# Optimization experiments

Measured on AMD Instinct MI355X. Metric: run time of the kernel, lower is better.

## Reference

```python
import jax, jax.numpy as jnp
import numpy as np
from jax import lax

N = 4096        # number of nodes (= number of hyperedges)
F_DIM = 256     # feature_dim
E_DIM = 128     # embed_dim
K = 9           # hardcoded k_neig in forward


def setup_inputs() -> dict:
    key = jax.random.key(0)
    ks = jax.random.split(key, 10)
    x = jax.random.normal(ks[0], (N, F_DIM), jnp.float32)
    # distance/similarity matrix; continuous values avoid argsort tie ambiguity
    XY_Adj = jax.random.uniform(ks[1], (N, N), jnp.float32)

    def unif(k, shape, fan_out):  # torch HGNN_conv init: U(-1/sqrt(out), 1/sqrt(out))
        s = 1.0 / np.sqrt(fan_out)
        return jax.random.uniform(k, shape, jnp.float32, -s, s)

    W10 = unif(ks[2], (F_DIM, E_DIM), E_DIM); b10 = unif(ks[3], (E_DIM,), E_DIM)
    W11 = unif(ks[4], (E_DIM, E_DIM), E_DIM); b11 = unif(ks[5], (E_DIM,), E_DIM)
    W20 = unif(ks[6], (E_DIM, E_DIM), E_DIM); b20 = unif(ks[7], (E_DIM,), E_DIM)
    W21 = unif(ks[8], (E_DIM, F_DIM), F_DIM); b21 = unif(ks[9], (F_DIM,), F_DIM)
    return {"x": x, "XY_Adj": XY_Adj,
            "W10": W10, "b10": b10, "W11": W11, "b11": b11,
            "W20": W20, "b20": b20, "W21": W21, "b21": b21}


def _build_G(dis, k):
    """Vectorized construct_H_with_KNN_from_distance + _generate_G_from_H.
    Picks the k LARGEST entries per row (original does reversed argsort),
    forces the center node into its own hyperedge, builds binary H [N,N]
    (rows=nodes, cols=hyperedges), then G = DV^-1/2 H DE^-1 H^T DV^-1/2 (W=I)."""
    n = dis.shape[0]
    centers = jnp.arange(n)
    dis = jnp.where(jnp.eye(n, dtype=bool), 0.0, dis)  # zero the diagonal
    _, idx = lax.top_k(dis, k)                         # [N, k] descending per row
    has_center = (idx == centers[:, None]).any(axis=1)
    idx = idx.at[:, k - 1].set(jnp.where(has_center, idx[:, k - 1], centers))
    H = jnp.zeros((n, n), dis.dtype).at[idx, centers[:, None]].set(1.0)
    DV = H.sum(axis=1)                                 # node degrees (>=1)
    DE = H.sum(axis=0)                                 # hyperedge degrees (=k)
    dv2 = DV ** -0.5
    left = dv2[:, None] * H * (1.0 / DE)[None, :]      # DV^-1/2 H DE^-1
    G = left @ (H.T * dv2[None, :])                    # ... H^T DV^-1/2
    return G


def _hgnn(x, G, W1, b1, W2, b2):
    # HGNN: relu(G(xW1+b1)) -> dropout (identity in eval) -> G(hW2+b2)
    h = jax.nn.relu(G @ (x @ W1 + b1))
    return G @ (h @ W2 + b2)


def reference(x, XY_Adj, W10, b10, W11, b11, W20, b20, W21, b21):
    G = _build_G(XY_Adj, K)
    x1 = jax.nn.relu(_hgnn(x, G, W10, b10, W11, b11))
    x2 = jax.nn.relu(_hgnn(x1, G, W20, b20, W21, b21))
    return (x, x1, x2)
```

## Files before the change

### kernel.cpp

```cpp
#include <hip/hip_runtime.h>

#define N_NODES 4096
#define KNN 9
#define CAPS 128
#define CAPE 32
#define THRESH 0.99f
#define GEMMB 1024

__device__ __forceinline__ bool vi_greater(float av, int aj, float bv, int bj) {
  return (av > bv) || (av == bv && aj < bj);
}

__global__ __launch_bounds__(256) void s0_kernel(const float* __restrict__ x,
                                                 const float* __restrict__ adj,
                                                 const float* __restrict__ W10,
                                                 const float* __restrict__ b10,
                                                 float* __restrict__ P,
                                                 float* __restrict__ xcopy,
                                                 int* __restrict__ cur,
                                                 int* __restrict__ idx) {
  __shared__ float sf[1024];
  __shared__ int   si[512];
  const int tid = threadIdx.x;

  if (blockIdx.x < GEMMB) {
    const int lane = tid & 63, wv = tid >> 6;
    const int row = blockIdx.x * 4 + wv;
    const float4* r4 = reinterpret_cast<const float4*>(adj + (size_t)row * N_NODES);
    float* wval = sf + wv * CAPS;
    int*   widx = si + wv * CAPS;
    const unsigned long long lmask = (1ull << lane) - 1;

    int n = 0;
#pragma unroll 4
    for (int t = 0; t < 16; ++t) {
      float4 f4 = r4[t * 64 + lane];
      float vals[4] = {f4.x, f4.y, f4.z, f4.w};
      int cb = (t * 64 + lane) * 4;
#pragma unroll
      for (int q = 0; q < 4; ++q) {
        bool pred = (vals[q] > THRESH);
        unsigned long long m = __ballot(pred);
        if (pred) {
          int p = n + __popcll(m & lmask);
          if (p < CAPS) { wval[p] = vals[q]; widx[p] = cb + q; }
        }
        n += __popcll(m);
      }
    }

    if (n >= 9 && n <= CAPS) {
      bool val0 = lane < n, val1 = lane + 64 < n;
      float v0 = 0.f, v1 = 0.f; int c0 = -1, c1 = -1;
      if (val0) { v0 = wval[lane];      c0 = widx[lane]; }
      if (val1) { v1 = wval[lane + 64]; c1 = widx[lane + 64]; }
      if (c0 == row) val0 = false;
      if (c1 == row) val1 = false;
      int r0 = 0, r1 = 0;
      if (n <= 64) {
        for (int s = 0; s < n; ++s) {
          float vs = wval[s]; int cs = widx[s];
          if (cs != row && vi_greater(vs, cs, v0, c0)) ++r0;
        }
      } else {
        for (int s = 0; s < n; ++s) {
          float vs = wval[s]; int cs = widx[s];
          bool d = (cs != row);
          if (d && vi_greater(vs, cs, v0, c0)) ++r0;
          if (d && vi_greater(vs, cs, v1, c1)) ++r1;
        }
      }
      if (val0 && r0 < 8) idx[row * KNN + r0] = c0;
      if (val1 && r1 < 8) idx[row * KNN + r1] = c1;
      if (lane == 0)      idx[row * KNN + 8] = row;
    } else {
      const float* r = adj + (size_t)row * N_NODES;
      float v[9]; int ji[9];
#pragma unroll
      for (int t = 0; t < 9; ++t) { v[t] = -3.0e38f; ji[t] = 0x7fffffff; }
      for (int t = 0; t < 64; ++t) {
        int cc = t * 64 + lane;
        float val = (cc == row) ? 0.0f : r[cc];
        if (vi_greater(val, cc, v[8], ji[8])) {
          v[8] = val; ji[8] = cc;
#pragma unroll
          for (int s = 8; s > 0; --s) {
            if (vi_greater(v[s], ji[s], v[s-1], ji[s-1])) {
              float tv = v[s]; v[s] = v[s-1]; v[s-1] = tv;
              int tj = ji[s]; ji[s] = ji[s-1]; ji[s-1] = tj;
            }
          }
        }
      }
      int o0=0,o1=0,o2=0,o3=0,o4=0,o5=0,o6=0,o7=0,o8=0;
      bool has_center = false;
#pragma unroll
      for (int rnd = 0; rnd < 9; ++rnd) {
        float mv = v[0]; int mj = ji[0];
#pragma unroll
        for (int d = 1; d < 64; d <<= 1) {
          float ov = __shfl_xor(mv, d);
          int   oj = __shfl_xor(mj, d);
          if (vi_greater(ov, oj, mv, mj)) { mv = ov; mj = oj; }
        }
        switch (rnd) {
          case 0: o0 = mj; break; case 1: o1 = mj; break;
          case 2: o2 = mj; break; case 3: o3 = mj; break;
          case 4: o4 = mj; break; case 5: o5 = mj; break;
          case 6: o6 = mj; break; case 7: o7 = mj; break;
          default: o8 = mj; break;
        }
        has_center = has_center || (mj == row);
        if (ji[0] == mj) {
#pragma unroll
          for (int s = 0; s < 8; ++s) { v[s] = v[s+1]; ji[s] = ji[s+1]; }
          v[8] = -3.0e38f; ji[8] = 0x7fffffff;
        }
      }
      if (!has_center) o8 = row;
      if (lane == 0) {
        int* ip = idx + row * KNN;
        ip[0]=o0; ip[1]=o1; ip[2]=o2; ip[3]=o3; ip[4]=o4;
        ip[5]=o5; ip[6]=o6; ip[7]=o7; ip[8]=o8;
      }
    }
  } else {
    int bb0 = blockIdx.x - GEMMB;
    int gid = bb0 * 256 + tid;
    if (gid < N_NODES) cur[gid] = 0;
    int m0 = bb0 * 4;
    {
      float4 y4 = reinterpret_cast<const float4*>(x + (size_t)m0 * 256)[tid];
      reinterpret_cast<float4*>(sf)[tid] = y4;
      reinterpret_cast<float4*>(xcopy + (size_t)m0 * 256)[tid] = y4;
    }
    __syncthreads();
    const int f  = tid & 127;
    const int rb = (tid >> 7) * 2;
    float a0 = 0.f, a1 = 0.f;
    for (int k = 0; k < 256; k += 4) {
      float w0 = W10[(k + 0) * 128 + f];
      float w1 = W10[(k + 1) * 128 + f];
      float w2 = W10[(k + 2) * 128 + f];
      float w3 = W10[(k + 3) * 128 + f];
      float4 y0 = *reinterpret_cast<const float4*>(&sf[(rb + 0) * 256 + k]);
      float4 y1 = *reinterpret_cast<const float4*>(&sf[(rb + 1) * 256 + k]);
      a0 = fmaf(y0.x, w0, fmaf(y0.y, w1, fmaf(y0.z, w2, fmaf(y0.w, w3, a0))));
      a1 = fmaf(y1.x, w0, fmaf(y1.y, w1, fmaf(y1.z, w2, fmaf(y1.w, w3, a1))));
    }
    float bb = b10[f];
    P[(size_t)(m0 + rb + 0) * 128 + f] = a0 + bb;
    P[(size_t)(m0 + rb + 1) * 128 + f] = a1 + bb;
  }
}

__global__ void build_elist(const int* __restrict__ idx, int* __restrict__ cur,
                            int* __restrict__ elist) {
  int t = blockIdx.x * blockDim.x + threadIdx.x;
  if (t >= N_NODES * KNN) return;
  int node = idx[t];
  int p = atomicAdd(&cur[node], 1);
  if (p < CAPE) elist[node * CAPE + p] = t / KNN;
}

template<int F>
__global__ __launch_bounds__(F) void edge_gather(const float* __restrict__ Y,
                                                 const int* __restrict__ idx,
                                                 const int* __restrict__ DV,
                                                 float* __restrict__ Z) {
  __shared__ int er[KNN];
  __shared__ float ew[KNN];
  int e = blockIdx.x;
  if (threadIdx.x < KNN) {
    int r = idx[e * KNN + threadIdx.x];
    er[threadIdx.x] = r;
    ew[threadIdx.x] = rsqrtf((float)DV[r]);
  }
  __syncthreads();
  int f = threadIdx.x;
  float acc = 0.f;
#pragma unroll
  for (int j = 0; j < KNN; ++j)
    acc = fmaf(ew[j], Y[(size_t)er[j] * F + f], acc);
  Z[(size_t)e * F + f] = acc * (1.0f / 9.0f);
}

template<int KD>
__device__ __forceinline__ float node_acc(const float* __restrict__ Z,
                                          const int* __restrict__ elist,
                                          int i, int f, int cnt) {
  const int4* el4 = reinterpret_cast<const int4*>(elist + i * CAPE);
  int4 ea = el4[0], eb = el4[1], ec = el4[2], ed = el4[3];
  int e1[16] = {ea.x, ea.y, ea.z, ea.w, eb.x, eb.y, eb.z, eb.w,
                ec.x, ec.y, ec.z, ec.w, ed.x, ed.y, ed.z, ed.w};
  float acc = 0.f;
#pragma unroll
  for (int j = 0; j < 16; ++j) {
    float m = (j < cnt) ? 1.0f : 0.0f;
    acc = fmaf(m, Z[(size_t)(e1[j] & (N_NODES - 1)) * KD + f], acc);
  }
  for (int t = 16; t < cnt; ++t)
    acc += Z[(size_t)elist[i * CAPE + t] * KD + f];
  return acc;
}

template<int F>
__global__ __launch_bounds__(F) void node_gather(const float* __restrict__ Z,
                                                 const int* __restrict__ elist,
                                                 const int* __restrict__ DV,
                                                 float* __restrict__ out) {
  int i = blockIdx.x;
  int f = threadIdx.x;
  int cnt = DV[i]; if (cnt > CAPE) cnt = CAPE;
  float acc = node_acc<F>(Z, elist, i, f, cnt);
  out[(size_t)i * F + f] = fmaxf(acc * rsqrtf((float)DV[i]), 0.f);
}

template<int FO, bool WRITE_H>
__global__ __launch_bounds__(256) void node_gemm(const float* __restrict__ Z,
                                                 const int* __restrict__ elist,
                                                 const int* __restrict__ DV,
                                                 const float* __restrict__ W,
                                                 const float* __restrict__ bias,
                                                 float* __restrict__ P,
                                                 float* __restrict__ Hout) {
  constexpr int KD = 128;
  constexpr int ROWS = 4;
  constexpr int RPT = (FO == 128) ? 2 : 4;
  __shared__ float ylds[ROWS * KD];
  int m0 = blockIdx.x * ROWS;
#pragma unroll
  for (int c0 = 0; c0 < ROWS * KD; c0 += 256) {
    int cell = c0 + threadIdx.x;
    int rr = cell >> 7, f = cell & 127;
    int i = m0 + rr;
    int cnt = DV[i]; if (cnt > CAPE) cnt = CAPE;
    float acc = node_acc<KD>(Z, elist, i, f, cnt);
    acc = fmaxf(acc * rsqrtf((float)DV[i]), 0.f);
    ylds[cell] = acc;
    if (WRITE_H) Hout[(size_t)i * KD + f] = acc;
  }
  __syncthreads();
  const int f  = (FO == 128) ? (threadIdx.x & 127) : threadIdx.x;
  const int rb = (FO == 128) ? ((threadIdx.x >> 7) * 2) : 0;
  float acc[RPT];
#pragma unroll
  for (int rr = 0; rr < RPT; ++rr) acc[rr] = 0.f;
  for (int k = 0; k < KD; k += 4) {
    float w0 = W[(size_t)(k + 0) * FO + f];
    float w1 = W[(size_t)(k + 1) * FO + f];
    float w2 = W[(size_t)(k + 2) * FO + f];
    float w3 = W[(size_t)(k + 3) * FO + f];
#pragma unroll
    for (int rr = 0; rr < RPT; ++rr) {
      float4 y = *reinterpret_cast<const float4*>(&ylds[(rb + rr) * KD + k]);
      acc[rr] = fmaf(y.x, w0, fmaf(y.y, w1, fmaf(y.z, w2, fmaf(y.w, w3, acc[rr]))));
    }
  }
  float bb = bias[f];
#pragma unroll
  for (int rr = 0; rr < RPT; ++rr)
    P[(size_t)(m0 + rb + rr) * FO + f] = acc[rr] + bb;
}

extern "C" void kernel_launch(void* const* d_in, const int* in_sizes, int n_in,
                              void* d_out, int out_size, void* d_ws, size_t ws_size,
                              hipStream_t stream) {
  const float* x   = (const float*)d_in[0];
  const float* adj = (const float*)d_in[1];
  const float* W10 = (const float*)d_in[2];
  const float* b10 = (const float*)d_in[3];
  const float* W11 = (const float*)d_in[4];
  const float* b11 = (const float*)d_in[5];
  const float* W20 = (const float*)d_in[6];
  const float* b20 = (const float*)d_in[7];
  const float* W21 = (const float*)d_in[8];
  const float* b21 = (const float*)d_in[9];
  float* out = (float*)d_out;

  char* w = (char*)d_ws;
  int*   idx   = (int*)(w + 0);
  int*   cur   = (int*)(w + 147456);
  int*   elist = (int*)(w + 163840);
  float* bufP  = (float*)(w + 688128);
  float* bufZ  = (float*)(w + 4882432);

  float* x1out = out + (size_t)N_NODES * 256;
  float* x2out = x1out + (size_t)N_NODES * 128;

  s0_kernel<<<2 * GEMMB, 256, 0, stream>>>(x, adj, W10, b10, bufP, out, cur, idx);
  build_elist<<<(N_NODES * KNN + 255) / 256, 256, 0, stream>>>(idx, cur, elist);

  edge_gather<128><<<N_NODES, 128, 0, stream>>>(bufP, idx, cur, bufZ);
  node_gemm<128, false><<<N_NODES / 4, 256, 0, stream>>>(bufZ, elist, cur,
                                                         W11, b11, bufP, nullptr);
  edge_gather<128><<<N_NODES, 128, 0, stream>>>(bufP, idx, cur, bufZ);
  node_gemm<128, true><<<N_NODES / 4, 256, 0, stream>>>(bufZ, elist, cur,
                                                        W20, b20, bufP, x1out);
  edge_gather<128><<<N_NODES, 128, 0, stream>>>(bufP, idx, cur, bufZ);
  node_gemm<256, false><<<N_NODES / 4, 256, 0, stream>>>(bufZ, elist, cur,
                                                         W21, b21, bufP, nullptr);
  edge_gather<256><<<N_NODES, 256, 0, stream>>>(bufP, idx, cur, bufZ);
  node_gather<256><<<N_NODES, 256, 0, stream>>>(bufZ, elist, cur, x2out);
}
```

Measured before the change: 89.80 us.

## Split each top-k row across four waves of a block instead of one wave

The top-k stage now assigns one adjacency row per 256-thread block, with each of the four waves scanning a quarter of the row and compacting above-threshold candidates into a per-wave 32-slot shared segment. Candidates from all segments are then ranked together using one thread per candidate. The goal is to shorten the serial per-row scan latency and raise memory-level parallelism by using four times as many blocks. The cost is a block barrier, smaller per-segment capacity (so the fallback path triggers more often if any quarter holds more than 32 candidates), and a fallback that runs on a single wave while the other three sit idle.

Measured after the change: 101.2 us. +12.7%, slower.

```diff
diff --git a/kernel.cpp b/kernel.cpp
--- a/kernel.cpp
+++ b/kernel.cpp
@@ -2,10 +2,9 @@
 
 #define N_NODES 4096
 #define KNN 9
-#define CAPS 128
 #define CAPE 32
 #define THRESH 0.99f
-#define GEMMB 1024
+#define TOPKB 4096
 
 __device__ __forceinline__ bool vi_greater(float av, int aj, float bv, int bj) {
   return (av > bv) || (av == bv && aj < bj);
@@ -20,60 +19,64 @@
                                                  int* __restrict__ cur,
                                                  int* __restrict__ idx) {
   __shared__ float sf[1024];
-  __shared__ int   si[512];
+  __shared__ int   si[128];
+  __shared__ int   scnt[4];
   const int tid = threadIdx.x;
 
-  if (blockIdx.x < GEMMB) {
+  if (blockIdx.x < TOPKB) {
     const int lane = tid & 63, wv = tid >> 6;
-    const int row = blockIdx.x * 4 + wv;
+    const int row = blockIdx.x;
     const float4* r4 = reinterpret_cast<const float4*>(adj + (size_t)row * N_NODES);
-    float* wval = sf + wv * CAPS;
-    int*   widx = si + wv * CAPS;
     const unsigned long long lmask = (1ull << lane) - 1;
+    float* wval = sf;
+    int*   widx = si;
 
     int n = 0;
-#pragma unroll 4
-    for (int t = 0; t < 16; ++t) {
-      float4 f4 = r4[t * 64 + lane];
+#pragma unroll
+    for (int t = 0; t < 4; ++t) {
+      float4 f4 = r4[wv * 256 + t * 64 + lane];
       float vals[4] = {f4.x, f4.y, f4.z, f4.w};
-      int cb = (t * 64 + lane) * 4;
+      int cb = (wv * 256 + t * 64 + lane) * 4;
 #pragma unroll
       for (int q = 0; q < 4; ++q) {
         bool pred = (vals[q] > THRESH);
         unsigned long long m = __ballot(pred);
         if (pred) {
           int p = n + __popcll(m & lmask);
-          if (p < CAPS) { wval[p] = vals[q]; widx[p] = cb + q; }
+          if (p < 32) { wval[wv * 32 + p] = vals[q]; widx[wv * 32 + p] = cb + q; }
         }
         n += __popcll(m);
       }
     }
-
-    if (n >= 9 && n <= CAPS) {
-      bool val0 = lane < n, val1 = lane + 64 < n;
-      float v0 = 0.f, v1 = 0.f; int c0 = -1, c1 = -1;
-      if (val0) { v0 = wval[lane];      c0 = widx[lane]; }
-      if (val1) { v1 = wval[lane + 64]; c1 = widx[lane + 64]; }
-      if (c0 == row) val0 = false;
-      if (c1 == row) val1 = false;
-      int r0 = 0, r1 = 0;
-      if (n <= 64) {
-        for (int s = 0; s < n; ++s) {
-          float vs = wval[s]; int cs = widx[s];
+    if (lane == 0) scnt[wv] = n;
+    __syncthreads();
+
+    const int n0 = scnt[0], n1 = scnt[1], n2 = scnt[2], n3 = scnt[3];
+    const int ntot = n0 + n1 + n2 + n3;
+    const bool ok = (ntot >= 9) && (n0 <= 32) && (n1 <= 32) &&
+                    (n2 <= 32) && (n3 <= 32);
+    if (ok) {
+      float v0 = 0.f; int c0 = -1; bool val0 = false;
+      if (tid < 128) {
+        int seg = tid >> 5, off = tid & 31;
+        if (off < scnt[seg]) {
+          v0 = wval[tid]; c0 = widx[tid];
+          val0 = (c0 != row);
+        }
+      }
+      int r0 = 0;
+#pragma unroll
+      for (int seg = 0; seg < 4; ++seg) {
+        int ns = scnt[seg];
+        int b = seg * 32;
+        for (int s = 0; s < ns; ++s) {
+          float vs = wval[b + s]; int cs = widx[b + s];
           if (cs != row && vi_greater(vs, cs, v0, c0)) ++r0;
         }
-      } else {
-        for (int s = 0; s < n; ++s) {
-          float vs = wval[s]; int cs = widx[s];
-          bool d = (cs != row);
-          if (d && vi_greater(vs, cs, v0, c0)) ++r0;
-          if (d && vi_greater(vs, cs, v1, c1)) ++r1;
-        }
       }
       if (val0 && r0 < 8) idx[row * KNN + r0] = c0;
-      if (val1 && r1 < 8) idx[row * KNN + r1] = c1;
-      if (lane == 0)      idx[row * KNN + 8] = row;
-    } else {
+      if (tid == 0)       idx[row * KNN + 8] = row;
+    } else if (wv == 0) {
       const float* r = adj + (size_t)row * N_NODES;
       float v[9]; int ji[9];
 #pragma unroll
@@ -125,7 +128,7 @@
       }
     }
   } else {
-    int bb0 = blockIdx.x - GEMMB;
+    int bb0 = blockIdx.x - TOPKB;
     int gid = bb0 * 256 + tid;
     if (gid < N_NODES) cur[gid] = 0;
     int m0 = bb0 * 4;
@@ -288,7 +291,7 @@
   float* x1out = out + (size_t)N_NODES * 256;
   float* x2out = x1out + (size_t)N_NODES * 128;
 
-  s0_kernel<<<2 * GEMMB, 256, 0, stream>>>(x, adj, W10, b10, bufP, out, cur, idx);
+  s0_kernel<<<TOPKB + 1024, 256, 0, stream>>>(x, adj, W10, b10, bufP, out, cur, idx);
   build_elist<<<(N_NODES * KNN + 255) / 256, 256, 0, stream>>>(idx, cur, elist);
 
   edge_gather<128><<<N_NODES, 128, 0, stream>>>(bufP, idx, cur, bufZ);
```
